# Kernel optimization log

Hardware: AMD Instinct MI355X
Metric: run time of the kernel (lower is better)

The kernel has to match this reference:

```python
import jax, jax.numpy as jnp
import numpy as np

N_FFT = 512
HOP = N_FFT // 4  # torch.stft default hop_length
TWO_PI = 2.0 * np.pi


def _stft_phase(x):
    """torch.stft(x, n_fft=512, return_complex=True) phase: center reflect-pad,
    rectangular window, onesided rfft. Returns [F, T'] with F = n_fft//2+1."""
    pad = N_FFT // 2
    xp = jnp.pad(x, (pad, pad), mode='reflect')
    n_frames = (xp.shape[0] - N_FFT) // HOP + 1
    idx = (np.arange(n_frames, dtype=np.int32)[:, None] * HOP
           + np.arange(N_FFT, dtype=np.int32)[None, :])
    frames = xp[idx]                      # [T', n_fft]
    spec = jnp.fft.rfft(frames, axis=-1)  # [T', F]
    return jnp.angle(spec).T              # [F, T']


def _anti_wrap(x):
    return jnp.abs(x - jnp.round(x / TWO_PI) * TWO_PI)


def _gd(p):
    # banded matmul with gd_matrix == out[f] = p[f-1] - p[f], out[0] = -p[0]
    return jnp.concatenate([-p[:1], p[:-1] - p[1:]], axis=0)


def _iaf(p):
    # banded matmul with iaf_matrix along time axis
    return jnp.concatenate([-p[:, :1], p[:, :-1] - p[:, 1:]], axis=1)


def setup_inputs() -> dict:
    key = jax.random.key(0)
    k1, k2 = jax.random.split(key)
    T = 4194304  # 2^22 samples (~262 s @ 16 kHz)
    yd = jax.random.normal(k1, (T,), dtype=jnp.float32)
    td = jax.random.normal(k2, (T,), dtype=jnp.float32)
    return {"yd": yd, "td": td}


def reference(yd, td):
    pr = _stft_phase(yd)  # [F, T']
    pg = _stft_phase(td)
    ip_loss = jnp.mean(_anti_wrap(pr - pg))
    gd_loss = jnp.mean(_anti_wrap(_gd(pr) - _gd(pg)))
    iaf_loss = jnp.mean(_anti_wrap(_iaf(pr) - _iaf(pg)))
    return (ip_loss, gd_loss, iaf_loss)
```

## Files before the change

### kernel.cpp

```cpp
#include <hip/hip_runtime.h>
#include <math.h>

#define HOP     128
#define NSLOTS  256
#define FPW     4
#define PI_F    3.14159265358979323846f
#define PI2_F   1.57079632679489661923f
#define K8      0.70710678118654752440f

#define LDS_FENCE() do { __asm__ volatile("" ::: "memory"); \
                         __builtin_amdgcn_wave_barrier(); } while (0)

struct cpx { float x, y; };
__device__ __forceinline__ cpx cadd(cpx a, cpx b){ return {a.x+b.x, a.y+b.y}; }
__device__ __forceinline__ cpx csub(cpx a, cpx b){ return {a.x-b.x, a.y-b.y}; }
__device__ __forceinline__ cpx cmul(cpx a, cpx b){
    return {fmaf(a.x,b.x,-a.y*b.y), fmaf(a.x,b.y, a.y*b.x)};
}
__device__ __forceinline__ cpx cmulc(cpx a, cpx b){
    return {fmaf(a.x,b.x, a.y*b.y), fmaf(a.y,b.x,-a.x*b.y)};
}

__device__ __forceinline__ float abs_angle(float re, float im) {
    float a = fabsf(im), b = fabsf(re);
    float mn = fminf(a, b), mx = fmaxf(a, b);
    float t = __fdividef(mn, fmaxf(mx, 1e-37f));
    float t2 = t * t;
    float p = fmaf(t2, -0.0117212f, 0.05265332f);
    p = fmaf(t2, p, -0.11643287f);
    p = fmaf(t2, p, 0.19354346f);
    p = fmaf(t2, p, -0.33262347f);
    p = fmaf(t2, p, 0.99997726f);
    float r = t * p;
    r = (a > b) ? (PI2_F - r) : r;
    r = (re < 0.f) ? (PI_F - r) : r;
    return r;
}

__device__ __forceinline__ void dft8(cpx v[8]) {
    cpx a0=cadd(v[0],v[4]), a1=cadd(v[1],v[5]), a2=cadd(v[2],v[6]), a3=cadd(v[3],v[7]);
    cpx b0=csub(v[0],v[4]), b1=csub(v[1],v[5]), b2=csub(v[2],v[6]), b3=csub(v[3],v[7]);
    b1 = cpx{K8*(b1.x+b1.y), K8*(b1.y-b1.x)};
    b2 = cpx{b2.y, -b2.x};
    b3 = cpx{K8*(b3.y-b3.x), -K8*(b3.x+b3.y)};
    cpx c0=cadd(a0,a2), c2=csub(a0,a2);
    cpx c1=cadd(a1,a3), c3=csub(a1,a3); c3 = cpx{c3.y, -c3.x};
    cpx d0=cadd(b0,b2), d2=csub(b0,b2);
    cpx d1=cadd(b1,b3), d3=csub(b1,b3); d3 = cpx{d3.y, -d3.x};
    v[0]=cadd(c0,c1); v[4]=csub(c0,c1);
    v[2]=cadd(c2,c3); v[6]=csub(c2,c3);
    v[1]=cadd(d0,d1); v[5]=csub(d0,d1);
    v[3]=cadd(d2,d3); v[7]=csub(d2,d3);
}

__global__ __launch_bounds__(256, 4) void phase_loss_kernel(
        const float* __restrict__ y, const float* __restrict__ g,
        float* __restrict__ acc, int* __restrict__ ticket,
        float* __restrict__ out, int T, int n_frames, float inv_count) {
    __shared__ float2 xch_all[4][576];
    __shared__ float2 tw2_lds[56];
    __shared__ float wsum[3][4];
    __shared__ int is_last;

    const int tid  = threadIdx.x;
    const int lane = tid & 63;
    const int wid  = tid >> 6;
    float2* xch = xch_all[wid];

    if (tid < 56) {
        int p = tid & 7, kk = tid >> 3;
        float ang = -(2.0f * PI_F / 64.0f) * (float)(p * (kk + 1));
        float sn, cs;
        __sincosf(ang, &sn, &cs);
        tw2_lds[tid] = make_float2(cs, sn);
    }

    cpx tw1[7];
    #pragma unroll
    for (int k = 1; k < 8; ++k) {
        float a1 = -(2.0f * PI_F / 512.0f) * (float)(lane * k);
        __sincosf(a1, &tw1[k-1].y, &tw1[k-1].x);
    }
    __syncthreads();

    float ip = 0.f, gd = 0.f, iaf = 0.f;
    cpx Cp[5];
    const int tmax_int = (T - 256) / HOP;
    const int l8 = lane & 7;

    auto herm_to_C = [&](float2 zk, float2 zn) -> cpx {
        float ur = zk.x + zn.x, ui = zk.y - zn.y;
        float vx = zk.x - zn.x, vy = zk.y + zn.y;
        return cpx{fmaf(ur, vy, -ui * vx),
                   fmaf(ur, vx,  ui * vy)};
    };

    auto do_frame = [&](int t, bool accum, bool hp) {
        cpx v[8];
        const int base = t * HOP - 256 + lane;
        if (t >= 2 && t <= tmax_int) {
            #pragma unroll
            for (int r = 0; r < 8; ++r) {
                int j = base + r * 64;
                v[r].x = y[j]; v[r].y = g[j];
            }
        } else {
            #pragma unroll
            for (int r = 0; r < 8; ++r) {
                int j = base + r * 64;
                j = (j < 0) ? -j : j;
                j = (j >= T) ? (2 * T - 2 - j) : j;
                v[r].x = y[j]; v[r].y = g[j];
            }
        }
        dft8(v);
        #pragma unroll
        for (int k = 1; k < 8; ++k) v[k] = cmul(v[k], tw1[k-1]);
        LDS_FENCE();
        #pragma unroll
        for (int k = 0; k < 8; ++k)
            xch[k * 72 + lane] = make_float2(v[k].x, v[k].y);
        LDS_FENCE();
        {
            const int ra = (lane >> 3) * 72 + l8;
            #pragma unroll
            for (int r = 0; r < 8; ++r) {
                float2 tmp = xch[ra + r * 8];
                v[r] = cpx{tmp.x, tmp.y};
            }
        }
        dft8(v);
        #pragma unroll
        for (int k = 1; k < 8; ++k) {
            float2 t2 = tw2_lds[((k - 1) << 3) + l8];
            v[k] = cmul(v[k], cpx{t2.x, t2.y});
        }
        LDS_FENCE();
        #pragma unroll
        for (int k = 0; k < 8; ++k)
            xch[k * 65 + lane] = make_float2(v[k].x, v[k].y);
        LDS_FENCE();
        {
            const int ra = (lane >> 3) * 65 + l8 * 8;
            #pragma unroll
            for (int r = 0; r < 8; ++r) {
                float2 tmp = xch[ra + r];
                v[r] = cpx{tmp.x, tmp.y};
            }
        }
        dft8(v);
        float2* Z = xch;
        LDS_FENCE();
        #pragma unroll
        for (int j = 0; j < 8; ++j)
            Z[lane + (j << 6)] = make_float2(v[j].x, v[j].y);
        LDS_FENCE();
        #pragma unroll
        for (int jj = 0; jj < 5; ++jj) {
            const int f = lane + (jj << 6);
            cpx cc = herm_to_C(make_float2(v[jj].x, v[jj].y),
                               Z[(512 - f) & 511]);
            if (accum && (jj < 4 || lane == 0)) {
                float aw = abs_angle(cc.x, cc.y);
                ip += aw;
                cpx cm = herm_to_C(Z[(f - 1) & 511], Z[(513 - f) & 511]);
                cpx qg = cmulc(cm, cc);
                gd += (f == 0) ? aw : abs_angle(qg.x, qg.y);
                if (hp) {
                    cpx qi = cmulc(Cp[jj], cc);
                    iaf += abs_angle(qi.x, qi.y);
                } else {
                    iaf += aw;
                }
            }
            Cp[jj] = cc;
        }
    };

    const int chain   = (blockIdx.x << 2) | wid;
    const int nchains = (int)(gridDim.x << 2);
    const int t0 = chain * FPW;
    int tend = t0 + FPW;
    if (chain == nchains - 1) tend = n_frames;
    const bool havep = (t0 > 0);

    if (havep) do_frame(t0 - 1, false, false);
    #pragma unroll 1
    for (int t = t0; t < tend; ++t)
        do_frame(t, true, havep || (t > t0));

    __syncthreads();
    for (int off = 32; off; off >>= 1) {
        ip  += __shfl_down(ip, off);
        gd  += __shfl_down(gd, off);
        iaf += __shfl_down(iaf, off);
    }
    if (lane == 0) { wsum[0][wid] = ip; wsum[1][wid] = gd; wsum[2][wid] = iaf; }
    __syncthreads();
    if (tid == 0) {
        const int slot = (int)(blockIdx.x & (NSLOTS - 1));
        atomicAdd(acc + 0 * NSLOTS + slot, wsum[0][0] + wsum[0][1] + wsum[0][2] + wsum[0][3]);
        atomicAdd(acc + 1 * NSLOTS + slot, wsum[1][0] + wsum[1][1] + wsum[1][2] + wsum[1][3]);
        atomicAdd(acc + 2 * NSLOTS + slot, wsum[2][0] + wsum[2][1] + wsum[2][2] + wsum[2][3]);
        __threadfence();
        is_last = (atomicAdd(ticket, 1) == (int)gridDim.x - 1);
    }
    __syncthreads();
    if (is_last) {
        for (int l = 0; l < 3; l++) {
            float vv = __hip_atomic_load(acc + l * NSLOTS + tid,
                                         __ATOMIC_RELAXED, __HIP_MEMORY_SCOPE_AGENT);
            for (int off = 32; off; off >>= 1) vv += __shfl_down(vv, off);
            if (lane == 0) wsum[l][wid] = vv;
        }
        __syncthreads();
        if (tid < 3)
            out[tid] = (wsum[tid][0] + wsum[tid][1] + wsum[tid][2] + wsum[tid][3]) * inv_count;
    }
}

extern "C" void kernel_launch(void* const* d_in, const int* in_sizes, int n_in,
                              void* d_out, int out_size, void* d_ws, size_t ws_size,
                              hipStream_t stream) {
    const float* y = (const float*)d_in[0];
    const float* g = (const float*)d_in[1];
    float* out = (float*)d_out;
    float* acc = (float*)d_ws;
    int* ticket = (int*)((char*)d_ws + 3 * NSLOTS * sizeof(float));
    const int T = in_sizes[0];
    const int n_frames = T / HOP + 1;
    int n_blocks = n_frames / (FPW * 4);
    if (n_blocks < 1) n_blocks = 1;

    hipMemsetAsync(d_ws, 0, 3 * NSLOTS * sizeof(float) + sizeof(int), stream);
    const float inv_count = 1.0f / (257.0f * (float)n_frames);
    phase_loss_kernel<<<n_blocks, 256, 0, stream>>>(y, g, acc, ticket, out,
                                                    T, n_frames, inv_count);
}
```

Before: 146.7 us.

## Halve per-wave LDS exchange buffer by splitting FFT transposes into two passes

The per-wave LDS scratch shrinks from 576 to 272 float2 entries. Each FFT transpose and the final spectrum exchange are now done in two half-size passes, with lanes 0-31 and 32-63 taking turns reading. The point is to cut shared-memory use per block so more blocks fit on a CU. In exchange each frame gets extra wave barriers and LDS round trips, half the lanes sit idle during each read phase, and the Hermitian edge cases (bins 0, 1 and 256) need special handling.

```diff
diff --git a/kernel.cpp b/kernel.cpp
--- a/kernel.cpp
+++ b/kernel.cpp
@@ -57,7 +57,7 @@
         const float* __restrict__ y, const float* __restrict__ g,
         float* __restrict__ acc, int* __restrict__ ticket,
         float* __restrict__ out, int T, int n_frames, float inv_count) {
-    __shared__ float2 xch_all[4][576];
+    __shared__ float2 xch_all[4][272];
     __shared__ float2 tw2_lds[56];
     __shared__ float wsum[3][4];
     __shared__ int is_last;
@@ -74,7 +74,6 @@
         __sincosf(ang, &sn, &cs);
         tw2_lds[tid] = make_float2(cs, sn);
     }
-
     cpx tw1[7];
     #pragma unroll
     for (int k = 1; k < 8; ++k) {
@@ -87,6 +86,7 @@
     cpx Cp[5];
     const int tmax_int = (T - 256) / HOP;
     const int l8 = lane & 7;
+    const int row = lane >> 3;
 
     auto herm_to_C = [&](float2 zk, float2 zn) -> cpx {
         float ur = zk.x + zn.x, ui = zk.y - zn.y;
@@ -116,19 +116,31 @@
         dft8(v);
         #pragma unroll
         for (int k = 1; k < 8; ++k) v[k] = cmul(v[k], tw1[k-1]);
-        LDS_FENCE();
-        #pragma unroll
-        for (int k = 0; k < 8; ++k)
-            xch[k * 72 + lane] = make_float2(v[k].x, v[k].y);
-        LDS_FENCE();
-        {
-            const int ra = (lane >> 3) * 72 + l8;
-            #pragma unroll
-            for (int r = 0; r < 8; ++r) {
-                float2 tmp = xch[ra + r * 8];
-                v[r] = cpx{tmp.x, tmp.y};
-            }
-        }
+        cpx u[4];
+        LDS_FENCE();
+        #pragma unroll
+        for (int k = 0; k < 4; ++k) xch[k * 68 + lane] = make_float2(v[k].x, v[k].y);
+        LDS_FENCE();
+        if (lane < 32) {
+            const int ra = row * 68 + l8;
+            #pragma unroll
+            for (int r = 0; r < 4; ++r) { float2 w = xch[ra + r * 8];       v[r] = cpx{w.x, w.y}; }
+            #pragma unroll
+            for (int r = 0; r < 4; ++r) { float2 w = xch[ra + (r + 4) * 8]; u[r] = cpx{w.x, w.y}; }
+        }
+        LDS_FENCE();
+        #pragma unroll
+        for (int k = 0; k < 4; ++k) xch[k * 68 + lane] = make_float2(v[k + 4].x, v[k + 4].y);
+        LDS_FENCE();
+        if (lane >= 32) {
+            const int ra = (row - 4) * 68 + l8;
+            #pragma unroll
+            for (int r = 0; r < 4; ++r) { float2 w = xch[ra + r * 8];       v[r] = cpx{w.x, w.y}; }
+            #pragma unroll
+            for (int r = 0; r < 4; ++r) { float2 w = xch[ra + (r + 4) * 8]; u[r] = cpx{w.x, w.y}; }
+        }
+        #pragma unroll
+        for (int r = 0; r < 4; ++r) v[r + 4] = u[r];
         dft8(v);
         #pragma unroll
         for (int k = 1; k < 8; ++k) {
@@ -137,43 +149,84 @@
         }
         LDS_FENCE();
         #pragma unroll
-        for (int k = 0; k < 8; ++k)
-            xch[k * 65 + lane] = make_float2(v[k].x, v[k].y);
-        LDS_FENCE();
-        {
-            const int ra = (lane >> 3) * 65 + l8 * 8;
-            #pragma unroll
-            for (int r = 0; r < 8; ++r) {
-                float2 tmp = xch[ra + r];
-                v[r] = cpx{tmp.x, tmp.y};
-            }
-        }
+        for (int k = 0; k < 4; ++k) xch[k * 67 + lane] = make_float2(v[k].x, v[k].y);
+        LDS_FENCE();
+        if (lane < 32) {
+            const int ra = row * 67 + l8 * 8;
+            #pragma unroll
+            for (int r = 0; r < 4; ++r) { float2 w = xch[ra + r];     v[r] = cpx{w.x, w.y}; }
+            #pragma unroll
+            for (int r = 0; r < 4; ++r) { float2 w = xch[ra + r + 4]; u[r] = cpx{w.x, w.y}; }
+        }
+        LDS_FENCE();
+        #pragma unroll
+        for (int k = 0; k < 4; ++k) xch[k * 67 + lane] = make_float2(v[k + 4].x, v[k + 4].y);
+        LDS_FENCE();
+        if (lane >= 32) {
+            const int ra = (row - 4) * 67 + l8 * 8;
+            #pragma unroll
+            for (int r = 0; r < 4; ++r) { float2 w = xch[ra + r];     v[r] = cpx{w.x, w.y}; }
+            #pragma unroll
+            for (int r = 0; r < 4; ++r) { float2 w = xch[ra + r + 4]; u[r] = cpx{w.x, w.y}; }
+        }
+        #pragma unroll
+        for (int r = 0; r < 4; ++r) v[r + 4] = u[r];
         dft8(v);
-        float2* Z = xch;
-        LDS_FENCE();
-        #pragma unroll
-        for (int j = 0; j < 8; ++j)
-            Z[lane + (j << 6)] = make_float2(v[j].x, v[j].y);
-        LDS_FENCE();
-        #pragma unroll
-        for (int jj = 0; jj < 5; ++jj) {
-            const int f = lane + (jj << 6);
-            cpx cc = herm_to_C(make_float2(v[jj].x, v[jj].y),
-                               Z[(512 - f) & 511]);
-            if (accum && (jj < 4 || lane == 0)) {
+        LDS_FENCE();
+        #pragma unroll
+        for (int j = 0; j < 4; ++j) xch[lane + (j << 6)] = make_float2(v[j].x, v[j].y);
+        LDS_FENCE();
+        float2 Q1[4], q255, q257;
+        if (accum) {
+            Q1[0] = xch[lane ? (lane - 1) : 0];
+            #pragma unroll
+            for (int j = 1; j < 4; ++j) Q1[j] = xch[lane + (j << 6) - 1];
+            if (lane == 0) q255 = xch[255];
+        }
+        LDS_FENCE();
+        #pragma unroll
+        for (int j = 0; j < 4; ++j) xch[lane + (j << 6)] = make_float2(v[j + 4].x, v[j + 4].y);
+        LDS_FENCE();
+        if (accum && lane == 0) q257 = xch[1];
+        #pragma unroll
+        for (int j = 0; j < 4; ++j) {
+            const int f = lane + (j << 6);
+            float2 zn = xch[256 - f];
+            if (j == 0 && lane == 0) zn = make_float2(v[0].x, v[0].y);
+            cpx cc = herm_to_C(make_float2(v[j].x, v[j].y), zn);
+            if (accum) {
                 float aw = abs_angle(cc.x, cc.y);
                 ip += aw;
-                cpx cm = herm_to_C(Z[(f - 1) & 511], Z[(513 - f) & 511]);
+                float2 q3 = xch[257 - f];
+                if (j == 0 && lane == 1) q3 = Q1[0];
+                cpx cm = herm_to_C(Q1[j], q3);
                 cpx qg = cmulc(cm, cc);
                 gd += (f == 0) ? aw : abs_angle(qg.x, qg.y);
                 if (hp) {
-                    cpx qi = cmulc(Cp[jj], cc);
+                    cpx qi = cmulc(Cp[j], cc);
                     iaf += abs_angle(qi.x, qi.y);
                 } else {
                     iaf += aw;
                 }
             }
-            Cp[jj] = cc;
+            Cp[j] = cc;
+        }
+        {
+            cpx cc = herm_to_C(make_float2(v[4].x, v[4].y), make_float2(v[4].x, v[4].y));
+            if (accum && lane == 0) {
+                float aw = abs_angle(cc.x, cc.y);
+                ip += aw;
+                cpx cm = herm_to_C(q255, q257);
+                cpx qg = cmulc(cm, cc);
+                gd += abs_angle(qg.x, qg.y);
+                if (hp) {
+                    cpx qi = cmulc(Cp[4], cc);
+                    iaf += abs_angle(qi.x, qi.y);
+                } else {
+                    iaf += aw;
+                }
+            }
+            Cp[4] = cc;
         }
     };
 
```

Result: no change. 146.0 us (-0.4%).
